# Optimization experiments

Measured on AMD Instinct MI355X. Metric: run time of the kernel, lower is better.

The kernel has to match this reference:

```python
import jax, jax.numpy as jnp
import numpy as np

B, S, FEAT, DK = 128, 2048, 512, 64

def setup_inputs() -> dict:
    key = jax.random.key(0)
    k1, k2, k3, k4, k5 = jax.random.split(key, 5)
    input_k = jax.random.normal(k1, (B, S, FEAT), dtype=jnp.float32)
    input_q = jax.random.normal(k2, (B, FEAT), dtype=jnp.float32)
    context_len = jax.random.randint(k3, (B,), 0, S + 1, dtype=jnp.int32)
    # Linear weights stored as [in, out] so y = x @ W
    W_K = jax.random.normal(k4, (FEAT, DK), dtype=jnp.float32) / np.sqrt(FEAT)
    W_Q = jax.random.normal(k5, (FEAT, DK), dtype=jnp.float32) / np.sqrt(FEAT)
    return {"input_k": input_k, "input_q": input_q, "context_len": context_len,
            "W_K": W_K, "W_Q": W_Q}

def reference(input_k, input_q, context_len, W_K, W_Q):
    # K: [B,S,dk], q: [B,dk]
    K = jnp.einsum('bsf,fd->bsd', input_k, W_K)
    q = input_q @ W_Q
    scores = jnp.einsum('bd,bsd->bs', q, K)  # [B,S] (n_heads=1, no scaling in original)
    mask = jnp.arange(S)[None, :] < context_len[:, None]  # [B,S]
    attn = jax.nn.softmax(jnp.where(mask, scores, -1e30), axis=-1)  # [B,S]
    context = jnp.einsum('bs,bsf->bf', attn, input_k)  # [B,FEAT]
    # length==0 rows produce zeros in the original
    context = jnp.where((context_len > 0)[:, None], context, 0.0)
    return context
```

## Files before the change

### kernel.cpp

```cpp
#include <hip/hip_runtime.h>
#include <math.h>

#define B_    128
#define S_    2048
#define FEAT_ 512
#define DK_   64
#define NSPLIT 16
#define CHUNK  (S_ / NSPLIT)

__global__ __launch_bounds__(256) void qv_kernel(
    const float* __restrict__ input_q, const float* __restrict__ W_Q,
    const float* __restrict__ W_K, float* __restrict__ v) {
  int b = blockIdx.x;
  int tid = threadIdx.x;
  __shared__ float xq[FEAT_];
  __shared__ float qs[DK_];
  for (int f = tid; f < FEAT_; f += 256) xq[f] = input_q[b * FEAT_ + f];
  __syncthreads();
  if (tid < DK_) {
    float s = 0.f;
    for (int f = 0; f < FEAT_; ++f) s += xq[f] * W_Q[f * DK_ + tid];
    qs[tid] = s;
  }
  __syncthreads();
  for (int f = tid; f < FEAT_; f += 256) {
    float s = 0.f;
#pragma unroll
    for (int d = 0; d < DK_; ++d) s += W_K[f * DK_ + d] * qs[d];
    v[b * FEAT_ + f] = s;
  }
}

__global__ __launch_bounds__(256) void pass_kernel(
    const float* __restrict__ input_k, const int* __restrict__ ctx,
    const float* __restrict__ v, float* __restrict__ pm,
    float* __restrict__ pl, float* __restrict__ pacc) {
  int split = blockIdx.x;
  int b = blockIdx.y;
  int L = ctx[b];
  int s0 = split * CHUNK;
  int s1 = min(s0 + CHUNK, L);
  int tid = threadIdx.x, wave = tid >> 6, lane = tid & 63;

  const float* vb = v + b * FEAT_;
  float4 v0 = *(const float4*)(vb + lane * 4);
  float4 v1 = *(const float4*)(vb + 256 + lane * 4);

  float m = -INFINITY, l = 0.f;
  float4 a0 = make_float4(0.f, 0.f, 0.f, 0.f);
  float4 a1 = make_float4(0.f, 0.f, 0.f, 0.f);

  for (int s = s0 + wave; s < s1; s += 4) {
    const float* row = input_k + ((size_t)b * S_ + s) * FEAT_;
    float4 x0 = *(const float4*)(row + lane * 4);
    float4 x1 = *(const float4*)(row + 256 + lane * 4);
    float p = x0.x * v0.x + x0.y * v0.y + x0.z * v0.z + x0.w * v0.w +
              x1.x * v1.x + x1.y * v1.y + x1.z * v1.z + x1.w * v1.w;
#pragma unroll
    for (int off = 32; off; off >>= 1) p += __shfl_xor(p, off, 64);
    float mn = fmaxf(m, p);
    float sc = __expf(m - mn);
    float w  = __expf(p - mn);
    l = l * sc + w;
    a0.x = fmaf(a0.x, sc, w * x0.x);
    a0.y = fmaf(a0.y, sc, w * x0.y);
    a0.z = fmaf(a0.z, sc, w * x0.z);
    a0.w = fmaf(a0.w, sc, w * x0.w);
    a1.x = fmaf(a1.x, sc, w * x1.x);
    a1.y = fmaf(a1.y, sc, w * x1.y);
    a1.z = fmaf(a1.z, sc, w * x1.z);
    a1.w = fmaf(a1.w, sc, w * x1.w);
    m = mn;
  }

  __shared__ float sm[4], sl[4];
  __shared__ float sa[4][FEAT_];
  if (lane == 0) { sm[wave] = m; sl[wave] = l; }
  *(float4*)&sa[wave][lane * 4] = a0;
  *(float4*)&sa[wave][256 + lane * 4] = a1;
  __syncthreads();

  float M = fmaxf(fmaxf(sm[0], sm[1]), fmaxf(sm[2], sm[3]));
  int idx = b * NSPLIT + split;
  if (M == -INFINITY) {
    if (tid == 0) { pm[idx] = -INFINITY; pl[idx] = 0.f; }
    for (int f = tid; f < FEAT_; f += 256) pacc[(size_t)idx * FEAT_ + f] = 0.f;
    return;
  }
  float e0 = __expf(sm[0] - M), e1 = __expf(sm[1] - M);
  float e2 = __expf(sm[2] - M), e3 = __expf(sm[3] - M);
  if (tid == 0) {
    pm[idx] = M;
    pl[idx] = e0 * sl[0] + e1 * sl[1] + e2 * sl[2] + e3 * sl[3];
  }
  for (int f = tid; f < FEAT_; f += 256)
    pacc[(size_t)idx * FEAT_ + f] =
        e0 * sa[0][f] + e1 * sa[1][f] + e2 * sa[2][f] + e3 * sa[3][f];
}

__global__ __launch_bounds__(256) void combine_kernel(
    const float* __restrict__ pm, const float* __restrict__ pl,
    const float* __restrict__ pacc, float* __restrict__ out) {
  int b = blockIdx.x;
  int tid = threadIdx.x;
  __shared__ float e[NSPLIT];
  __shared__ float inv_s;
  if (tid == 0) {
    float M = -INFINITY;
    for (int i = 0; i < NSPLIT; ++i) M = fmaxf(M, pm[b * NSPLIT + i]);
    float lt = 0.f;
    for (int i = 0; i < NSPLIT; ++i) {
      float ei = (M == -INFINITY) ? 0.f : __expf(pm[b * NSPLIT + i] - M);
      e[i] = ei;
      lt += ei * pl[b * NSPLIT + i];
    }
    inv_s = (lt > 0.f) ? 1.f / lt : 0.f;
  }
  __syncthreads();
  float inv = inv_s;
  for (int f = tid; f < FEAT_; f += 256) {
    float s = 0.f;
#pragma unroll
    for (int i = 0; i < NSPLIT; ++i)
      s += e[i] * pacc[((size_t)(b * NSPLIT + i)) * FEAT_ + f];
    out[b * FEAT_ + f] = s * inv;
  }
}

extern "C" void kernel_launch(void* const* d_in, const int* in_sizes, int n_in,
                              void* d_out, int out_size, void* d_ws, size_t ws_size,
                              hipStream_t stream) {
  const float* input_k = (const float*)d_in[0];
  const float* input_q = (const float*)d_in[1];
  const int*   ctx     = (const int*)d_in[2];
  const float* W_K     = (const float*)d_in[3];
  const float* W_Q     = (const float*)d_in[4];
  float* out = (float*)d_out;

  char* ws = (char*)d_ws;
  float* v    = (float*)ws;
  float* pm   = (float*)(ws + (size_t)B_ * FEAT_ * sizeof(float));
  float* pl   = pm + B_ * NSPLIT;
  float* pacc = pl + B_ * NSPLIT;

  qv_kernel<<<B_, 256, 0, stream>>>(input_q, W_Q, W_K, v);
  pass_kernel<<<dim3(NSPLIT, B_), 256, 0, stream>>>(input_k, ctx, v, pm, pl, pacc);
  combine_kernel<<<B_, 256, 0, stream>>>(pm, pl, pacc, out);
}
```

Before: 77.04 us.

## Unroll pass loop over four rows, double splits, parallelize q projection and combine

The main pass kernel now processes four rows per wave per iteration, issuing eight float4 loads before the reductions so more memory traffic is in flight and the online-softmax rescale runs once per four rows. NSPLIT grows from 16 to 32, doubling the number of blocks to improve occupancy for short contexts, at the cost of more partial results for the combine step. The q projection is split across all 256 threads with float4 W_K loads, and the combine max/sum now uses a warp shuffle reduction instead of a serial loop. These changes raise register use and add some combine traffic in return for better latency hiding.

```diff
diff --git a/kernel.cpp b/kernel.cpp
--- a/kernel.cpp
+++ b/kernel.cpp
@@ -5,7 +5,7 @@
 #define S_    2048
 #define FEAT_ 512
 #define DK_   64
-#define NSPLIT 16
+#define NSPLIT 32
 #define CHUNK  (S_ / NSPLIT)
 
 __global__ __launch_bounds__(256) void qv_kernel(
@@ -14,21 +14,46 @@
   int b = blockIdx.x;
   int tid = threadIdx.x;
   __shared__ float xq[FEAT_];
+  __shared__ float part[4][DK_];
   __shared__ float qs[DK_];
   for (int f = tid; f < FEAT_; f += 256) xq[f] = input_q[b * FEAT_ + f];
   __syncthreads();
-  if (tid < DK_) {
+  {
+    int d = tid & 63, c = tid >> 6;
     float s = 0.f;
-    for (int f = 0; f < FEAT_; ++f) s += xq[f] * W_Q[f * DK_ + tid];
-    qs[tid] = s;
-  }
+    int f0 = c * 128;
+    for (int f = f0; f < f0 + 128; ++f) s = fmaf(xq[f], W_Q[f * DK_ + d], s);
+    part[c][d] = s;
+  }
+  __syncthreads();
+  if (tid < DK_)
+    qs[tid] = part[0][tid] + part[1][tid] + part[2][tid] + part[3][tid];
   __syncthreads();
   for (int f = tid; f < FEAT_; f += 256) {
+    const float4* wk = (const float4*)(W_K + f * DK_);
     float s = 0.f;
 #pragma unroll
-    for (int d = 0; d < DK_; ++d) s += W_K[f * DK_ + d] * qs[d];
+    for (int d4 = 0; d4 < DK_ / 4; ++d4) {
+      float4 w = wk[d4];
+      s = fmaf(w.x, qs[d4 * 4 + 0], s);
+      s = fmaf(w.y, qs[d4 * 4 + 1], s);
+      s = fmaf(w.z, qs[d4 * 4 + 2], s);
+      s = fmaf(w.w, qs[d4 * 4 + 3], s);
+    }
     v[b * FEAT_ + f] = s;
   }
+}
+
+__device__ __forceinline__ float dot8(float4 x0, float4 x1, float4 v0, float4 v1) {
+  float p = x0.x * v0.x;
+  p = fmaf(x0.y, v0.y, p);
+  p = fmaf(x0.z, v0.z, p);
+  p = fmaf(x0.w, v0.w, p);
+  p = fmaf(x1.x, v1.x, p);
+  p = fmaf(x1.y, v1.y, p);
+  p = fmaf(x1.z, v1.z, p);
+  p = fmaf(x1.w, v1.w, p);
+  return p;
 }
 
 __global__ __launch_bounds__(256) void pass_kernel(
@@ -50,26 +75,79 @@
   float4 a0 = make_float4(0.f, 0.f, 0.f, 0.f);
   float4 a1 = make_float4(0.f, 0.f, 0.f, 0.f);
 
-  for (int s = s0 + wave; s < s1; s += 4) {
-    const float* row = input_k + ((size_t)b * S_ + s) * FEAT_;
+  const float* base = input_k + (size_t)b * S_ * FEAT_;
+  int s = s0 + wave;
+
+  for (; s + 12 < s1; s += 16) {
+    const float* r0 = base + (size_t)s * FEAT_;
+    const float* r1 = r0 + 4 * FEAT_;
+    const float* r2 = r0 + 8 * FEAT_;
+    const float* r3 = r0 + 12 * FEAT_;
+    float4 x00 = *(const float4*)(r0 + lane * 4);
+    float4 x01 = *(const float4*)(r0 + 256 + lane * 4);
+    float4 x10 = *(const float4*)(r1 + lane * 4);
+    float4 x11 = *(const float4*)(r1 + 256 + lane * 4);
+    float4 x20 = *(const float4*)(r2 + lane * 4);
+    float4 x21 = *(const float4*)(r2 + 256 + lane * 4);
+    float4 x30 = *(const float4*)(r3 + lane * 4);
+    float4 x31 = *(const float4*)(r3 + 256 + lane * 4);
+
+    float p0 = dot8(x00, x01, v0, v1);
+    float p1 = dot8(x10, x11, v0, v1);
+    float p2 = dot8(x20, x21, v0, v1);
+    float p3 = dot8(x30, x31, v0, v1);
+#pragma unroll
+    for (int off = 32; off; off >>= 1) {
+      p0 += __shfl_xor(p0, off, 64);
+      p1 += __shfl_xor(p1, off, 64);
+      p2 += __shfl_xor(p2, off, 64);
+      p3 += __shfl_xor(p3, off, 64);
+    }
+    float mn = fmaxf(fmaxf(fmaxf(p0, p1), fmaxf(p2, p3)), m);
+    float sc = __expf(m - mn);
+    float w0 = __expf(p0 - mn), w1 = __expf(p1 - mn);
+    float w2 = __expf(p2 - mn), w3 = __expf(p3 - mn);
+    l = fmaf(l, sc, (w0 + w1) + (w2 + w3));
+#define ACC(comp, f0c, f1c, f2c, f3c)                       \
+    {                                                        \
+      float t = comp * sc;                                   \
+      t = fmaf(w0, f0c, t);                                  \
+      t = fmaf(w1, f1c, t);                                  \
+      t = fmaf(w2, f2c, t);                                  \
+      t = fmaf(w3, f3c, t);                                  \
+      comp = t;                                              \
+    }
+    ACC(a0.x, x00.x, x10.x, x20.x, x30.x)
+    ACC(a0.y, x00.y, x10.y, x20.y, x30.y)
+    ACC(a0.z, x00.z, x10.z, x20.z, x30.z)
+    ACC(a0.w, x00.w, x10.w, x20.w, x30.w)
+    ACC(a1.x, x01.x, x11.x, x21.x, x31.x)
+    ACC(a1.y, x01.y, x11.y, x21.y, x31.y)
+    ACC(a1.z, x01.z, x11.z, x21.z, x31.z)
+    ACC(a1.w, x01.w, x11.w, x21.w, x31.w)
+#undef ACC
+    m = mn;
+  }
+
+  for (; s < s1; s += 4) {
+    const float* row = base + (size_t)s * FEAT_;
     float4 x0 = *(const float4*)(row + lane * 4);
     float4 x1 = *(const float4*)(row + 256 + lane * 4);
-    float p = x0.x * v0.x + x0.y * v0.y + x0.z * v0.z + x0.w * v0.w +
-              x1.x * v1.x + x1.y * v1.y + x1.z * v1.z + x1.w * v1.w;
+    float p = dot8(x0, x1, v0, v1);
 #pragma unroll
     for (int off = 32; off; off >>= 1) p += __shfl_xor(p, off, 64);
     float mn = fmaxf(m, p);
     float sc = __expf(m - mn);
-    float w  = __expf(p - mn);
-    l = l * sc + w;
-    a0.x = fmaf(a0.x, sc, w * x0.x);
-    a0.y = fmaf(a0.y, sc, w * x0.y);
-    a0.z = fmaf(a0.z, sc, w * x0.z);
-    a0.w = fmaf(a0.w, sc, w * x0.w);
-    a1.x = fmaf(a1.x, sc, w * x1.x);
-    a1.y = fmaf(a1.y, sc, w * x1.y);
-    a1.z = fmaf(a1.z, sc, w * x1.z);
-    a1.w = fmaf(a1.w, sc, w * x1.w);
+    float w = __expf(p - mn);
+    l = fmaf(l, sc, w);
+    a0.x = fmaf(w, x0.x, a0.x * sc);
+    a0.y = fmaf(w, x0.y, a0.y * sc);
+    a0.z = fmaf(w, x0.z, a0.z * sc);
+    a0.w = fmaf(w, x0.w, a0.w * sc);
+    a1.x = fmaf(w, x1.x, a1.x * sc);
+    a1.y = fmaf(w, x1.y, a1.y * sc);
+    a1.z = fmaf(w, x1.z, a1.z * sc);
+    a1.w = fmaf(w, x1.w, a1.w * sc);
     m = mn;
   }
 
@@ -105,16 +183,17 @@
   int tid = threadIdx.x;
   __shared__ float e[NSPLIT];
   __shared__ float inv_s;
-  if (tid == 0) {
-    float M = -INFINITY;
-    for (int i = 0; i < NSPLIT; ++i) M = fmaxf(M, pm[b * NSPLIT + i]);
-    float lt = 0.f;
-    for (int i = 0; i < NSPLIT; ++i) {
-      float ei = (M == -INFINITY) ? 0.f : __expf(pm[b * NSPLIT + i] - M);
-      e[i] = ei;
-      lt += ei * pl[b * NSPLIT + i];
-    }
-    inv_s = (lt > 0.f) ? 1.f / lt : 0.f;
+  if (tid < NSPLIT) {
+    float mi = pm[b * NSPLIT + tid];
+    float M = mi;
+#pragma unroll
+    for (int off = 16; off; off >>= 1) M = fmaxf(M, __shfl_xor(M, off, 64));
+    float ei = (M == -INFINITY) ? 0.f : __expf(mi - M);
+    e[tid] = ei;
+    float lw = ei * pl[b * NSPLIT + tid];
+#pragma unroll
+    for (int off = 16; off; off >>= 1) lw += __shfl_xor(lw, off, 64);
+    if (tid == 0) inv_s = (lw > 0.f) ? 1.f / lw : 0.f;
   }
   __syncthreads();
   float inv = inv_s;
@@ -122,7 +201,7 @@
     float s = 0.f;
 #pragma unroll
     for (int i = 0; i < NSPLIT; ++i)
-      s += e[i] * pacc[((size_t)(b * NSPLIT + i)) * FEAT_ + f];
+      s = fmaf(e[i], pacc[((size_t)(b * NSPLIT + i)) * FEAT_ + f], s);
     out[b * FEAT_ + f] = s * inv;
   }
 }
```

New measurement: 66.06 us. 1.17x faster.
